# Kernel tuning notes

Measured on AMD Instinct MI355X. Metric: run time of the kernel, lower is better.

The kernel has to match this reference:

```python
import jax, jax.numpy as jnp
import numpy as np

DIM = 192
NH = 6
HD = DIM // NH            # 32
SCALE = HD ** -0.5
HID = int(DIM * 4.0)      # 768
EPS = 1e-5


def _ln(x, g, b):
    m = jnp.mean(x, axis=-1, keepdims=True)
    v = jnp.mean((x - m) ** 2, axis=-1, keepdims=True)
    return (x - m) * jax.lax.rsqrt(v + EPS) * g + b


def setup_inputs() -> dict:
    key = jax.random.key(0)
    ks = jax.random.split(key, 6)
    H = W = T = 48
    B = 1
    L = H * W * T
    return {
        "x": jax.random.normal(ks[0], (B, L, DIM), jnp.float32),
        "norm1_g": jnp.ones((DIM,), jnp.float32),
        "norm1_b": jnp.zeros((DIM,), jnp.float32),
        "qkv_w": jax.random.normal(ks[1], (3 * DIM, DIM), jnp.float32) * 0.02,
        "qkv_b": jnp.zeros((3 * DIM,), jnp.float32),
        "proj_w": jax.random.normal(ks[2], (DIM, DIM), jnp.float32) * 0.02,
        "proj_b": jnp.zeros((DIM,), jnp.float32),
        "norm2_g": jnp.ones((DIM,), jnp.float32),
        "norm2_b": jnp.zeros((DIM,), jnp.float32),
        "fc1_w": jax.random.normal(ks[3], (HID, DIM), jnp.float32) * 0.02,
        "fc1_b": jnp.zeros((HID,), jnp.float32),
        "fc2_w": jax.random.normal(ks[4], (DIM, HID), jnp.float32) * 0.02,
        "fc2_b": jnp.zeros((DIM,), jnp.float32),
        "H": H, "W": W, "T": T,
    }


def reference(x, norm1_g, norm1_b, qkv_w, qkv_b, proj_w, proj_b,
              norm2_g, norm2_b, fc1_w, fc1_b, fc2_w, fc2_b, H, W, T):
    B, L, C = x.shape
    shortcut = x
    h = _ln(x, norm1_g, norm1_b)
    # axial_dims='12' -> extra_dim=3: permute to (B, T, H, W, C), attend over H*W
    h = h.reshape(B, H, W, T, C).transpose(0, 3, 1, 2, 4).reshape(B * T, H * W, C)
    B_, N, _ = h.shape
    qkv = h @ qkv_w.T + qkv_b                                   # (B_, N, 3C)
    # faithful reproduction of the module's unusual reshape mixing batch into head dim
    qkv = qkv.transpose(1, 0, 2).reshape(1, N, 3, NH, B_ * HD).transpose(2, 0, 3, 1, 4)
    q, k, v = qkv[0] * SCALE, qkv[1], qkv[2]                    # (1, NH, N, B_*HD)
    attn = jax.nn.softmax(jnp.einsum('ohnd,ohmd->ohnm', q, k), axis=-1)
    o = jnp.einsum('ohnm,ohmd->ohnd', attn, v)                  # (1, NH, N, B_*HD)
    o = o.transpose(0, 2, 1, 3).reshape(B_, N, C)
    o = o @ proj_w.T + proj_b
    o = o.reshape(B, H * W * T, C)                              # module does NOT undo the permute
    x1 = shortcut + o
    m = _ln(x1, norm2_g, norm2_b)
    m = jax.nn.gelu(m @ fc1_w.T + fc1_b, approximate=False) @ fc2_w.T + fc2_b
    return x1 + m
```

## Files before the change

kernel.cpp:

```cpp
#include <hip/hip_runtime.h>

typedef __bf16 bf16_t;
typedef __attribute__((ext_vector_type(8))) __bf16 bf16x8;
typedef __attribute__((ext_vector_type(4))) float f32x4;

__device__ __forceinline__ float gelu_exact(float x) {
    return 0.5f * x * (1.0f + erff(x * 0.70710678118654752f));
}

#define AS1 __attribute__((address_space(1)))
#define AS3 __attribute__((address_space(3)))

#define MM_HALF(IH)                                                            \
    __builtin_amdgcn_s_setprio(1);                                             \
    _Pragma("unroll")                                                          \
    for (int u = 0; u < 4; ++u) {                                              \
        _Pragma("unroll")                                                      \
        for (int j = 0; j < 4; ++j)                                            \
            acc[(IH) * 4 + u][j] = __builtin_amdgcn_mfma_f32_16x16x32_bf16(    \
                a[u], b[j], acc[(IH) * 4 + u][j], 0, 0, 0);                    \
    }                                                                          \
    __builtin_amdgcn_s_setprio(0);

#define MIDBAR()                                                \
    asm volatile("" ::: "memory");                              \
    __builtin_amdgcn_s_barrier();                               \
    asm volatile("s_waitcnt lgkmcnt(0)" ::: "memory");

#define ENDBAR()                                                \
    asm volatile("" ::: "memory");                              \
    __builtin_amdgcn_s_barrier();                               \
    asm volatile("" ::: "memory");

__global__ __launch_bounds__(512, 2)
void gemm256(const bf16_t* __restrict__ A, int lda, long aBatch,
             const bf16_t* __restrict__ B, int ldb, long bBatch,
             bf16_t* __restrict__ C, int ldc, long cBatch, int K)
{
    extern __shared__ __align__(16) bf16_t lds[];
    const int t    = threadIdx.x;
    const int w    = t >> 6;
    const int lane = t & 63;
    const int wm   = w >> 2, wn = w & 3;
    const int lrow = lane & 15;
    const int kq4  = lane >> 4;

    const unsigned gx = gridDim.x, gy = gridDim.y;
    unsigned nwg = gx * gy * gridDim.z;
    unsigned lin = (blockIdx.z * gy + blockIdx.y) * gx + blockIdx.x;
    {
        unsigned q = nwg >> 3, r = nwg & 7;
        unsigned xcd = lin & 7, idx = lin >> 3;
        lin = (xcd < r ? xcd * (q + 1) : r * (q + 1) + (xcd - r) * q) + idx;
    }
    const unsigned bx = lin % gx;
    const unsigned by = (lin / gx) % gy;
    const unsigned bz = lin / (gx * gy);

    const long n0 = (long)bx * 256;
    const long m0 = (long)by * 256;
    const bf16_t* Ap = A + (long)bz * aBatch + m0 * lda;
    const bf16_t* Bp = B + (long)bz * bBatch + n0 * ldb;
    C += (long)bz * cBatch;

    f32x4 acc[8][4] = {};

    auto stage_half = [&](int buf, int op, int kh, int kt) {
        const bf16_t* base = op ? Bp : Ap;
        const int ld = op ? ldb : lda;
        #pragma unroll
        for (int e = 0; e < 2; ++e) {
            const int row = e * 128 + (t >> 2);
            const int cw  = (t & 3) ^ ((row ^ (row >> 2)) & 3);
            const bf16_t* src = base + (long)row * ld + (kt * 64 + kh * 32 + cw * 8);
            __builtin_amdgcn_global_load_lds(
                (AS1 void*)(bf16_t*)src,
                (AS3 void*)(lds + buf * 32768 + op * 16384 + kh * 8192 + e * 4096 + w * 512),
                16, 0, 0);
        }
    };

    bf16x8 a[4], b[4];
    auto rdA = [&](int c, int ks, int ih) {
        #pragma unroll
        for (int u = 0; u < 4; ++u) {
            const int row = wm * 128 + (ih * 4 + u) * 16 + lrow;
            const int cw  = kq4 ^ ((row ^ (row >> 2)) & 3);
            a[u] = *(const bf16x8*)(lds + c * 32768 + ks * 8192 + row * 32 + cw * 8);
        }
    };
    auto rdB = [&](int c, int ks) {
        #pragma unroll
        for (int u = 0; u < 4; ++u) {
            const int row = wn * 64 + u * 16 + lrow;
            const int cw  = kq4 ^ ((row ^ (row >> 2)) & 3);
            b[u] = *(const bf16x8*)(lds + c * 32768 + 16384 + ks * 8192 + row * 32 + cw * 8);
        }
    };

    const int nt = K >> 6;
    stage_half(0, 1, 0, 0); stage_half(0, 0, 0, 0);
    stage_half(0, 1, 1, 0); stage_half(0, 0, 1, 0);
    if (nt > 1) {
        stage_half(1, 1, 0, 1); stage_half(1, 0, 0, 1); stage_half(1, 1, 1, 1);
        asm volatile("s_waitcnt vmcnt(6)" ::: "memory");
    } else {
        asm volatile("s_waitcnt vmcnt(0)" ::: "memory");
    }
    __builtin_amdgcn_s_barrier();
    asm volatile("" ::: "memory");

    for (int kt = 0; kt < nt; ++kt) {
        const int c = kt & 1;
        rdA(c, 0, 0); rdB(c, 0);
        if (kt + 1 < nt) stage_half(c ^ 1, 0, 1, kt + 1);
        MIDBAR(); MM_HALF(0); ENDBAR();
        rdA(c, 0, 1);
        if (kt + 2 < nt) stage_half(c, 1, 0, kt + 2);
        MIDBAR(); MM_HALF(1); ENDBAR();
        rdA(c, 1, 0); rdB(c, 1);
        if (kt + 2 < nt) stage_half(c, 0, 0, kt + 2);
        MIDBAR(); MM_HALF(0); ENDBAR();
        rdA(c, 1, 1);
        if (kt + 2 < nt) {
            stage_half(c, 1, 1, kt + 2);
            asm volatile("s_waitcnt vmcnt(6)" ::: "memory");
        } else {
            asm volatile("s_waitcnt vmcnt(0)" ::: "memory");
        }
        MIDBAR(); MM_HALF(1); ENDBAR();
    }

    const int ccol  = lane & 15;
    const int crow4 = (lane >> 4) * 4;
    #pragma unroll
    for (int i = 0; i < 8; ++i) {
        long rowb = m0 + wm * 128 + i * 16 + crow4;
        #pragma unroll
        for (int j = 0; j < 4; ++j) {
            long col = n0 + wn * 64 + j * 16 + ccol;
            #pragma unroll
            for (int r = 0; r < 4; ++r)
                C[(rowb + r) * ldc + col] = (bf16_t)acc[i][j][r];
        }
    }
}

template<int BM, int BN, int EPI, int SWZ>
__global__ __launch_bounds__(256)
void mgemm(const bf16_t* __restrict__ A, int lda, long aBatch,
           const bf16_t* __restrict__ B, int ldb, long bBatch,
           bf16_t* __restrict__ C, int ldc, long cBatch,
           const float* __restrict__ bias, int K,
           float* __restrict__ Cf, const float* __restrict__ resid)
{
    constexpr int MR = BM / 32;
    constexpr int NR = BN / 32;
    constexpr int LPT = BM / 32 + BN / 32;
    __shared__ __align__(16) bf16_t As[2][BM * 64];
    __shared__ __align__(16) bf16_t Bs[2][BN * 64];
    const int t    = threadIdx.x;
    const int w    = t >> 6;
    const int lane = t & 63;
    const int wr   = w >> 1, wc = w & 1;

    unsigned bx = blockIdx.x, by = blockIdx.y, bz = blockIdx.z;
    if constexpr (SWZ) {
        const unsigned gx = gridDim.x, gy = gridDim.y, gz = gridDim.z;
        unsigned lin = (bz * gy + by) * gx + bx;
        const unsigned cpx = (gx * gy * gz) >> 3;
        lin = (lin & 7) * cpx + (lin >> 3);
        bx = lin % gx; lin /= gx;
        by = lin % gy; bz = lin / gy;
    }

    const long n0 = (long)bx * BN;
    const long m0 = (long)by * BM;
    A += (long)bz * aBatch;
    B += (long)bz * bBatch;
    if constexpr (EPI != 3) C += (long)bz * cBatch;

    f32x4 acc[MR][NR] = {};

    const int srow8  = t >> 3;
    const int schunk = (t & 7) ^ (srow8 & 7);
    const int lrow = lane & 15;
    const int kq4  = lane >> 4;

    auto stage = [&](int buf, int k0) {
        #pragma unroll
        for (int c = 0; c < BM / 32; ++c) {
            const bf16_t* src = A + (m0 + c * 32 + srow8) * (long)lda + (k0 + schunk * 8);
            __builtin_amdgcn_global_load_lds(
                (AS1 void*)(bf16_t*)src,
                (AS3 void*)(As[buf] + c * 2048 + w * 512), 16, 0, 0);
        }
        #pragma unroll
        for (int c = 0; c < BN / 32; ++c) {
            const bf16_t* src = B + (n0 + c * 32 + srow8) * (long)ldb + (k0 + schunk * 8);
            __builtin_amdgcn_global_load_lds(
                (AS1 void*)(bf16_t*)src,
                (AS3 void*)(Bs[buf] + c * 2048 + w * 512), 16, 0, 0);
        }
    };

    const int nt = K >> 6;
    stage(0, 0);
    int cur = 0;
    for (int kt = 0; kt < nt; ++kt) {
        if (kt + 1 < nt) {
            stage(cur ^ 1, (kt + 1) << 6);
            if constexpr (LPT == 8)
                asm volatile("s_waitcnt vmcnt(8)" ::: "memory");
            else
                asm volatile("s_waitcnt vmcnt(6)" ::: "memory");
        } else {
            asm volatile("s_waitcnt vmcnt(0)" ::: "memory");
        }
        __builtin_amdgcn_s_barrier();

        bf16x8 af[MR][2], bfr[NR][2];
        #pragma unroll
        for (int i = 0; i < MR; ++i) {
            const int row = wr * (BM / 2) + i * 16 + lrow;
            #pragma unroll
            for (int ks = 0; ks < 2; ++ks) {
                const int ch = (ks * 4 + kq4) ^ (row & 7);
                af[i][ks] = *(const bf16x8*)(As[cur] + row * 64 + ch * 8);
            }
        }
        #pragma unroll
        for (int j = 0; j < NR; ++j) {
            const int row = wc * (BN / 2) + j * 16 + lrow;
            #pragma unroll
            for (int ks = 0; ks < 2; ++ks) {
                const int ch = (ks * 4 + kq4) ^ (row & 7);
                bfr[j][ks] = *(const bf16x8*)(Bs[cur] + row * 64 + ch * 8);
            }
        }
        #pragma unroll
        for (int ks = 0; ks < 2; ++ks)
            #pragma unroll
            for (int i = 0; i < MR; ++i)
                #pragma unroll
                for (int j = 0; j < NR; ++j)
                    acc[i][j] = __builtin_amdgcn_mfma_f32_16x16x32_bf16(
                        af[i][ks], bfr[j][ks], acc[i][j], 0, 0, 0);

        asm volatile("s_waitcnt lgkmcnt(0)" ::: "memory");
        __builtin_amdgcn_s_barrier();
        cur ^= 1;
    }

    const int ccol  = lane & 15;
    const int crow4 = (lane >> 4) * 4;
    #pragma unroll
    for (int i = 0; i < MR; ++i) {
        long rowb = m0 + wr * (BM / 2) + i * 16 + crow4;
        #pragma unroll
        for (int j = 0; j < NR; ++j) {
            long col = n0 + wc * (BN / 2) + j * 16 + ccol;
            #pragma unroll
            for (int r = 0; r < 4; ++r) {
                float v = acc[i][j][r];
                long row = rowb + r;
                if constexpr (EPI == 0) {
                    C[row * ldc + col] = (bf16_t)v;
                } else if constexpr (EPI == 1) {
                    C[row * ldc + col] = (bf16_t)(v + bias[col]);
                } else if constexpr (EPI == 2) {
                    C[row * ldc + col] = (bf16_t)gelu_exact(v + bias[col]);
                } else {
                    long idx = row * ldc + col;
                    Cf[idx] = resid[idx] + v + bias[col];
                }
            }
        }
    }
}

__global__ __launch_bounds__(256)
void transpose_v(const bf16_t* __restrict__ Y, bf16_t* __restrict__ Vt)
{
    __shared__ bf16_t tile[64][80];
    const int h  = blockIdx.z;
    const int e0 = blockIdx.x * 64;
    const int m0 = blockIdx.y * 64;
    const int t  = threadIdx.x;
    const int lr = t >> 3;
    const int lc8 = t & 7;

    #pragma unroll
    for (int i = 0; i < 64; i += 32) {
        int row = lr + i;
        bf16x8 vv = *(const bf16x8*)(Y + (long)(m0 + row) * 27648 + 18432 + h * 1536 + e0 + lc8 * 8);
        int cs = lc8 ^ (row >> 3);
        *(bf16x8*)&tile[row][cs * 8] = vv;
    }
    __syncthreads();
    #pragma unroll
    for (int i = 0; i < 64; i += 32) {
        int er = lr + i;
        bf16x8 vv;
        #pragma unroll
        for (int j = 0; j < 8; ++j) {
            int row = lc8 * 8 + j;
            int cs = (er >> 3) ^ lc8;
            vv[j] = tile[row][cs * 8 + (er & 7)];
        }
        *(bf16x8*)(Vt + ((long)h * 1536 + e0 + er) * 2304 + m0 + lc8 * 8) = vv;
    }
}

__global__ __launch_bounds__(256)
void ln_fast(const float* __restrict__ x, const float* __restrict__ g,
             const float* __restrict__ b, bf16_t* __restrict__ o, int nrows)
{
    const int lane = threadIdx.x & 63;
    const int wave = threadIdx.x >> 6;
    const float g0 = g[lane], g1 = g[lane + 64], g2 = g[lane + 128];
    const float b0 = b[lane], b1 = b[lane + 64], b2 = b[lane + 128];
    for (long row = (long)blockIdx.x * 4 + wave; row < nrows; row += (long)gridDim.x * 4) {
        const float* xr = x + row * 192;
        float v0 = xr[lane], v1 = xr[lane + 64], v2 = xr[lane + 128];
        float s  = v0 + v1 + v2;
        float ss = v0 * v0 + v1 * v1 + v2 * v2;
        #pragma unroll
        for (int d = 32; d > 0; d >>= 1) {
            s  += __shfl_xor(s, d);
            ss += __shfl_xor(ss, d);
        }
        float mean = s * (1.f / 192.f);
        float var  = ss * (1.f / 192.f) - mean * mean;
        float rs   = rsqrtf(var + 1e-5f);
        bf16_t* orow = o + row * 192;
        orow[lane]       = (bf16_t)((v0 - mean) * rs * g0 + b0);
        orow[lane + 64]  = (bf16_t)((v1 - mean) * rs * g1 + b1);
        orow[lane + 128] = (bf16_t)((v2 - mean) * rs * g2 + b2);
    }
}

__global__ __launch_bounds__(256)
void softmax_fast(bf16_t* __restrict__ S)
{
    const float SC = 0.17677669529663687f;
    __shared__ float wmax[4], wsum[4];
    const long base = (long)blockIdx.x * 2304;
    const int t = threadIdx.x;
    const int lane = t & 63, w = t >> 6;
    float v[9];
    float mx = -1e30f;
    #pragma unroll
    for (int i = 0; i < 9; ++i) {
        v[i] = (float)S[base + t + i * 256] * SC;
        mx = fmaxf(mx, v[i]);
    }
    #pragma unroll
    for (int d = 32; d > 0; d >>= 1) mx = fmaxf(mx, __shfl_xor(mx, d));
    if (lane == 0) wmax[w] = mx;
    __syncthreads();
    mx = fmaxf(fmaxf(wmax[0], wmax[1]), fmaxf(wmax[2], wmax[3]));
    float sum = 0.f;
    #pragma unroll
    for (int i = 0; i < 9; ++i) { v[i] = __expf(v[i] - mx); sum += v[i]; }
    #pragma unroll
    for (int d = 32; d > 0; d >>= 1) sum += __shfl_xor(sum, d);
    if (lane == 0) wsum[w] = sum;
    __syncthreads();
    const float inv = 1.f / (wsum[0] + wsum[1] + wsum[2] + wsum[3]);
    #pragma unroll
    for (int i = 0; i < 9; ++i) S[base + t + i * 256] = (bf16_t)(v[i] * inv);
}

__global__ __launch_bounds__(256)
void cast_all(const float* __restrict__ w0, const float* __restrict__ w1,
              const float* __restrict__ w2, const float* __restrict__ w3,
              bf16_t* __restrict__ o0, bf16_t* __restrict__ o1,
              bf16_t* __restrict__ o2, bf16_t* __restrict__ o3)
{
    int i = blockIdx.x * 256 + threadIdx.x;
    if (i < 110592)       o0[i] = (bf16_t)w0[i];
    else if (i < 147456)  o1[i - 110592] = (bf16_t)w1[i - 110592];
    else if (i < 294912)  o2[i - 147456] = (bf16_t)w2[i - 147456];
    else if (i < 442368)  o3[i - 294912] = (bf16_t)w3[i - 294912];
}

extern "C" void kernel_launch(void* const* d_in, const int* in_sizes, int n_in,
                              void* d_out, int out_size, void* d_ws, size_t ws_size,
                              hipStream_t stream)
{
    (void)in_sizes; (void)n_in; (void)out_size; (void)ws_size;
    const float* x      = (const float*)d_in[0];
    const float* n1g    = (const float*)d_in[1];
    const float* n1b    = (const float*)d_in[2];
    const float* qkv_w  = (const float*)d_in[3];
    const float* qkv_b  = (const float*)d_in[4];
    const float* proj_w = (const float*)d_in[5];
    const float* proj_b = (const float*)d_in[6];
    const float* n2g    = (const float*)d_in[7];
    const float* n2b    = (const float*)d_in[8];
    const float* fc1_w  = (const float*)d_in[9];
    const float* fc1_b  = (const float*)d_in[10];
    const float* fc2_w  = (const float*)d_in[11];
    const float* fc2_b  = (const float*)d_in[12];
    float* out = (float*)d_out;

    char* ws = (char*)d_ws;
    size_t off = 0;
    auto alloc = [&](size_t nbytes) -> void* {
        off = (off + 255) & ~(size_t)255;
        void* p = ws + off;
        off += nbytes;
        return p;
    };

    bf16_t* Wq   = (bf16_t*)alloc((size_t)576 * 192 * 2);
    bf16_t* Wp   = (bf16_t*)alloc((size_t)192 * 192 * 2);
    bf16_t* W1   = (bf16_t*)alloc((size_t)768 * 192 * 2);
    bf16_t* W2   = (bf16_t*)alloc((size_t)192 * 768 * 2);
    bf16_t* Hbuf = (bf16_t*)alloc((size_t)110592 * 192 * 2);
    bf16_t* Qkv  = (bf16_t*)alloc((size_t)110592 * 768 * 2);
    bf16_t* Vt   = Qkv + (size_t)110592 * 576;
    bf16_t* Sbuf = (bf16_t*)d_out;

    static bool attrOk = []() {
        return hipFuncSetAttribute(reinterpret_cast<const void*>(gemm256),
                                   hipFuncAttributeMaxDynamicSharedMemorySize,
                                   131072) == hipSuccess;
    }();

    cast_all<<<1728, 256, 0, stream>>>(qkv_w, proj_w, fc1_w, fc2_w, Wq, Wp, W1, W2);

    ln_fast<<<2048, 256, 0, stream>>>(x, n1g, n1b, Hbuf, 110592);
    mgemm<128, 64, 1, 0><<<dim3(9, 864, 1), 256, 0, stream>>>(
        Hbuf, 192, 0, Wq, 192, 0, Qkv, 576, 0, qkv_b, 192, nullptr, nullptr);
    transpose_v<<<dim3(24, 36, 6), 256, 0, stream>>>(Qkv, Vt);
    if (attrOk) {
        gemm256<<<dim3(9, 9, 6), 512, 131072, stream>>>(
            Qkv, 27648, 1536, Qkv + 9216, 27648, 1536,
            Sbuf, 2304, (long)2304 * 2304, 1536);
    } else {
        mgemm<128, 128, 0, 1><<<dim3(18, 18, 6), 256, 0, stream>>>(
            Qkv, 27648, 1536, Qkv + 9216, 27648, 1536,
            Sbuf, 2304, (long)2304 * 2304, nullptr, 1536, nullptr, nullptr);
    }
    softmax_fast<<<13824, 256, 0, stream>>>(Sbuf);
    if (attrOk) {
        gemm256<<<dim3(6, 9, 6), 512, 131072, stream>>>(
            Sbuf, 2304, (long)2304 * 2304, Vt, 2304, (long)1536 * 2304,
            Hbuf, 9216, 1536, 2304);
    } else {
        mgemm<128, 128, 0, 1><<<dim3(12, 18, 6), 256, 0, stream>>>(
            Sbuf, 2304, (long)2304 * 2304, Vt, 2304, (long)1536 * 2304,
            Hbuf, 9216, 1536, nullptr, 2304, nullptr, nullptr);
    }
    mgemm<128, 64, 3, 0><<<dim3(3, 864, 1), 256, 0, stream>>>(
        Hbuf, 192, 0, Wp, 192, 0, nullptr, 192, 0, proj_b, 192, out, x);
    ln_fast<<<2048, 256, 0, stream>>>(out, n2g, n2b, Hbuf, 110592);
    mgemm<128, 128, 2, 0><<<dim3(6, 864, 1), 256, 0, stream>>>(
        Hbuf, 192, 0, W1, 192, 0, Qkv, 768, 0, fc1_b, 192, nullptr, nullptr);
    mgemm<128, 64, 3, 0><<<dim3(3, 864, 1), 256, 0, stream>>>(
        Qkv, 768, 0, W2, 768, 0, nullptr, 192, 0, fc2_b, 768, out, out);
}
```

Before: 789.9 us.

## Restage gemm256 loads as full-K quarter tiles with single-stage prefetch

Changes the LDS layout of the 256-wide GEMM tile from two 32-wide K halves to full 64-wide rows with an XOR-by-row-mod-8 chunk swizzle. Global-to-LDS staging becomes row quarters covering the whole K slice. The prefetch schedule now loads the next K tile into the other buffer spread over the four sub-steps, instead of a two-deep lookahead, with vmcnt waits placed after the MFMA blocks. The goal is wider contiguous global reads and fewer LDS bank conflicts, at the cost of less prefetch distance.

```diff
diff --git a/kernel.cpp b/kernel.cpp
--- a/kernel.cpp
+++ b/kernel.cpp
@@ -39,8 +39,8 @@
 {
     extern __shared__ __align__(16) bf16_t lds[];
     const int t    = threadIdx.x;
+    const int lane = t & 63;
     const int w    = t >> 6;
-    const int lane = t & 63;
     const int wm   = w >> 2, wn = w & 3;
     const int lrow = lane & 15;
     const int kq4  = lane >> 4;
@@ -65,19 +65,16 @@
 
     f32x4 acc[8][4] = {};
 
-    auto stage_half = [&](int buf, int op, int kh, int kt) {
+    auto stage_q = [&](int buf, int op, int q, int kt) {
         const bf16_t* base = op ? Bp : Ap;
         const int ld = op ? ldb : lda;
-        #pragma unroll
-        for (int e = 0; e < 2; ++e) {
-            const int row = e * 128 + (t >> 2);
-            const int cw  = (t & 3) ^ ((row ^ (row >> 2)) & 3);
-            const bf16_t* src = base + (long)row * ld + (kt * 64 + kh * 32 + cw * 8);
-            __builtin_amdgcn_global_load_lds(
-                (AS1 void*)(bf16_t*)src,
-                (AS3 void*)(lds + buf * 32768 + op * 16384 + kh * 8192 + e * 4096 + w * 512),
-                16, 0, 0);
-        }
+        const int row = q * 64 + (t >> 3);
+        const int ch  = (t & 7) ^ (row & 7);
+        const bf16_t* src = base + (long)row * ld + (kt * 64 + ch * 8);
+        __builtin_amdgcn_global_load_lds(
+            (AS1 void*)(bf16_t*)src,
+            (AS3 void*)(lds + buf * 32768 + op * 16384 + q * 4096 + t * 8),
+            16, 0, 0);
     };
 
     bf16x8 a[4], b[4];
@@ -85,50 +82,48 @@
         #pragma unroll
         for (int u = 0; u < 4; ++u) {
             const int row = wm * 128 + (ih * 4 + u) * 16 + lrow;
-            const int cw  = kq4 ^ ((row ^ (row >> 2)) & 3);
-            a[u] = *(const bf16x8*)(lds + c * 32768 + ks * 8192 + row * 32 + cw * 8);
+            const int ch  = (ks * 4 + kq4) ^ (row & 7);
+            a[u] = *(const bf16x8*)(lds + c * 32768 + row * 64 + ch * 8);
         }
     };
     auto rdB = [&](int c, int ks) {
         #pragma unroll
         for (int u = 0; u < 4; ++u) {
             const int row = wn * 64 + u * 16 + lrow;
-            const int cw  = kq4 ^ ((row ^ (row >> 2)) & 3);
-            b[u] = *(const bf16x8*)(lds + c * 32768 + 16384 + ks * 8192 + row * 32 + cw * 8);
+            const int ch  = (ks * 4 + kq4) ^ (row & 7);
+            b[u] = *(const bf16x8*)(lds + c * 32768 + 16384 + row * 64 + ch * 8);
         }
     };
 
     const int nt = K >> 6;
-    stage_half(0, 1, 0, 0); stage_half(0, 0, 0, 0);
-    stage_half(0, 1, 1, 0); stage_half(0, 0, 1, 0);
-    if (nt > 1) {
-        stage_half(1, 1, 0, 1); stage_half(1, 0, 0, 1); stage_half(1, 1, 1, 1);
-        asm volatile("s_waitcnt vmcnt(6)" ::: "memory");
-    } else {
-        asm volatile("s_waitcnt vmcnt(0)" ::: "memory");
-    }
+    stage_q(0, 1, 0, 0); stage_q(0, 1, 1, 0); stage_q(0, 1, 2, 0); stage_q(0, 1, 3, 0);
+    stage_q(0, 0, 0, 0); stage_q(0, 0, 2, 0);
+    stage_q(0, 0, 1, 0); stage_q(0, 0, 3, 0);
+    asm volatile("s_waitcnt vmcnt(2)" ::: "memory");
     __builtin_amdgcn_s_barrier();
     asm volatile("" ::: "memory");
 
     for (int kt = 0; kt < nt; ++kt) {
         const int c = kt & 1;
+        const bool pf = (kt + 1 < nt);
         rdA(c, 0, 0); rdB(c, 0);
-        if (kt + 1 < nt) stage_half(c ^ 1, 0, 1, kt + 1);
-        MIDBAR(); MM_HALF(0); ENDBAR();
+        if (pf) { stage_q(c ^ 1, 1, 0, kt + 1); stage_q(c ^ 1, 1, 1, kt + 1); }
+        MIDBAR(); MM_HALF(0);
+        if (pf) asm volatile("s_waitcnt vmcnt(2)" ::: "memory");
+        else    asm volatile("s_waitcnt vmcnt(0)" ::: "memory");
+        ENDBAR();
         rdA(c, 0, 1);
-        if (kt + 2 < nt) stage_half(c, 1, 0, kt + 2);
+        if (pf) { stage_q(c ^ 1, 1, 2, kt + 1); stage_q(c ^ 1, 1, 3, kt + 1); }
         MIDBAR(); MM_HALF(1); ENDBAR();
         rdA(c, 1, 0); rdB(c, 1);
-        if (kt + 2 < nt) stage_half(c, 0, 0, kt + 2);
+        if (pf) { stage_q(c ^ 1, 0, 0, kt + 1); stage_q(c ^ 1, 0, 2, kt + 1); }
         MIDBAR(); MM_HALF(0); ENDBAR();
         rdA(c, 1, 1);
-        if (kt + 2 < nt) {
-            stage_half(c, 1, 1, kt + 2);
-            asm volatile("s_waitcnt vmcnt(6)" ::: "memory");
-        } else {
-            asm volatile("s_waitcnt vmcnt(0)" ::: "memory");
-        }
-        MIDBAR(); MM_HALF(1); ENDBAR();
+        if (pf) { stage_q(c ^ 1, 0, 1, kt + 1); stage_q(c ^ 1, 0, 3, kt + 1); }
+        MIDBAR(); MM_HALF(1);
+        if (pf) asm volatile("s_waitcnt vmcnt(2)" ::: "memory");
+        else    asm volatile("s_waitcnt vmcnt(0)" ::: "memory");
+        ENDBAR();
     }
 
     const int ccol  = lane & 15;
```

After: 773.5 us. 2.1% less time.
